# Optimization experiments

Measured on AMD Instinct MI355X. Metric: run time of the kernel, lower is better.

The kernel has to match this reference:

```python
import jax, jax.numpy as jnp
import numpy as np

B, E, F = 16384, 128, 6
ITEM_V, CATE_V, HIST = 91718, 11, 50
I_IDX, J_IDX = np.triu_indices(F, k=1)  # 15 field pairs, loop order (0,1),(0,2),...
EPS = 1e-5


def _xavier(key, shape):
    fan_in, fan_out = shape[0], shape[-1]
    std = (2.0 / (fan_in + fan_out)) ** 0.5
    return std * jax.random.normal(key, shape, dtype=jnp.float32)


def setup_inputs() -> dict:
    key = jax.random.key(0)
    ks = jax.random.split(key, 20)
    inp = {
        'item_id': jax.random.randint(ks[0], (B,), 0, ITEM_V),
        'item_emb_d128': jax.random.normal(ks[1], (B, 128), dtype=jnp.float32),
        'likes_level': jax.random.randint(ks[2], (B,), 0, CATE_V),
        'views_level': jax.random.randint(ks[3], (B,), 0, CATE_V),
        'item_seq': jax.random.randint(ks[4], (B, HIST), 0, ITEM_V),
        # learned parameters
        'item_emb': 0.05 * jax.random.normal(ks[5], (ITEM_V, E), dtype=jnp.float32),
        'cate_emb': 0.05 * jax.random.normal(ks[6], (CATE_V, E), dtype=jnp.float32),
        'mm_W': _xavier(ks[7], (128, E)), 'mm_b': jnp.zeros((E,), jnp.float32),
        'ln_g': jnp.ones((E,), jnp.float32), 'ln_b': jnp.zeros((E,), jnp.float32),
        'se_W1': _xavier(ks[8], (F, F // 2)), 'se_b1': jnp.zeros((F // 2,), jnp.float32),
        'se_W2': _xavier(ks[9], (F // 2, F)), 'se_b2': jnp.zeros((F,), jnp.float32),
        'bi_W': _xavier(ks[10], (E, E)),
        'mlp_W1': _xavier(ks[11], (21 * E, 512)), 'mlp_b1': jnp.zeros((512,), jnp.float32),
        'bn1_g': jnp.ones((512,), jnp.float32), 'bn1_b': jnp.zeros((512,), jnp.float32),
        'bn1_rm': jnp.zeros((512,), jnp.float32), 'bn1_rv': jnp.ones((512,), jnp.float32),
        'mlp_W2': _xavier(ks[12], (512, 256)), 'mlp_b2': jnp.zeros((256,), jnp.float32),
        'bn2_g': jnp.ones((256,), jnp.float32), 'bn2_b': jnp.zeros((256,), jnp.float32),
        'bn2_rm': jnp.zeros((256,), jnp.float32), 'bn2_rv': jnp.ones((256,), jnp.float32),
        'mlp_W3': _xavier(ks[13], (256, 1)), 'mlp_b3': jnp.zeros((1,), jnp.float32),
    }
    return inp


def _forward(item_id, item_emb_d128, likes_level, views_level, item_seq,
             item_emb, cate_emb, mm_W, mm_b, ln_g, ln_b,
             se_W1, se_b1, se_W2, se_b2, bi_W,
             mlp_W1, mlp_b1, bn1_g, bn1_b, bn1_rm, bn1_rv,
             mlp_W2, mlp_b2, bn2_g, bn2_b, bn2_rm, bn2_rv,
             mlp_W3, mlp_b3):
    b = item_id.shape[0]
    tab = item_emb.at[0].set(0.0)  # padding_idx=0
    like_feat = cate_emb[likes_level]
    view_feat = cate_emb[views_level]
    item_feat = tab[item_id]
    # mm_proj: Linear -> LayerNorm -> ReLU
    mm = item_emb_d128 @ mm_W + mm_b
    mu = mm.mean(-1, keepdims=True)
    var = jnp.var(mm, axis=-1, keepdims=True)
    mm = jax.nn.relu((mm - mu) / jnp.sqrt(var + EPS) * ln_g + ln_b)
    # masked mean pooling over history
    seq_emb = tab[item_seq]                               # (B, HIST, E)
    valid = (item_seq != 0).astype(seq_emb.dtype)
    seq_sum = (seq_emb * valid[..., None]).sum(1)
    cnt = jnp.clip(valid.sum(1, keepdims=True), 1.0)
    hist_feat = seq_sum / cnt
    user_feat = jnp.zeros((b, E), seq_emb.dtype)
    x = jnp.stack([user_feat, like_feat, view_feat, item_feat, mm, hist_feat], axis=1)  # (B,6,E)
    # SENet
    z = x.mean(-1)
    w = jax.nn.sigmoid(jax.nn.relu(z @ se_W1 + se_b1) @ se_W2 + se_b2)
    xs = x * w[:, :, None]
    # bilinear 'all'
    xw = jnp.einsum('bfe,ed->bfd', xs, bi_W)
    p = xs[:, I_IDX, :] * xw[:, J_IDX, :]                 # (B,15,E)
    c = jnp.concatenate([xs.reshape(b, -1), p.reshape(b, -1)], axis=1)  # (B, 2688)
    # MLP head (eval mode: BN uses running stats, dropout off)
    h = c @ mlp_W1 + mlp_b1
    h = jax.nn.relu((h - bn1_rm) / jnp.sqrt(bn1_rv + EPS) * bn1_g + bn1_b)
    h = h @ mlp_W2 + mlp_b2
    h = jax.nn.relu((h - bn2_rm) / jnp.sqrt(bn2_rv + EPS) * bn2_g + bn2_b)
    logits = h @ mlp_W3 + mlp_b3
    return jax.nn.sigmoid(logits)[:, 0]


def reference(item_id, item_emb_d128, likes_level, views_level, item_seq,
              item_emb, cate_emb, mm_W, mm_b, ln_g, ln_b,
              se_W1, se_b1, se_W2, se_b2, bi_W,
              mlp_W1, mlp_b1, bn1_g, bn1_b, bn1_rm, bn1_rv,
              mlp_W2, mlp_b2, bn2_g, bn2_b, bn2_rm, bn2_rv,
              mlp_W3, mlp_b3):
    return _forward(item_id, item_emb_d128, likes_level, views_level, item_seq,
                    item_emb, cate_emb, mm_W, mm_b, ln_g, ln_b,
                    se_W1, se_b1, se_W2, se_b2, bi_W,
                    mlp_W1, mlp_b1, bn1_g, bn1_b, bn1_rm, bn1_rv,
                    mlp_W2, mlp_b2, bn2_g, bn2_b, bn2_rm, bn2_rv,
                    mlp_W3, mlp_b3)
```

## Files before the change

kernel.cpp:

```cpp
#include <hip/hip_runtime.h>
#include <hip/hip_bf16.h>

typedef __hip_bfloat16 bfloat;
typedef __bf16 bf16x8 __attribute__((ext_vector_type(8)));
typedef float f32x4 __attribute__((ext_vector_type(4)));

#define B_SZ   16384
#define E_DIM  128
#define HIST_L 50


#define IPACK 0x3221110000ULL
#define JPACK 0x3323213210ULL

__device__ __forceinline__ void gl_lds16(const void* g, void* l) {
    __builtin_amdgcn_global_load_lds(
        (const __attribute__((address_space(1))) unsigned int*)g,
        (__attribute__((address_space(3))) unsigned int*)l, 16, 0, 0);
}

__device__ __forceinline__ bf16x8 mul_bf16x8(bf16x8 a, bf16x8 b) {
    union { bf16x8 v; __hip_bfloat162 h[4]; } ua, ub, ur;
    ua.v = a; ub.v = b;
    #pragma unroll
    for (int i = 0; i < 4; ++i) ur.h[i] = __hmul2(ua.h[i], ub.h[i]);
    return ur.v;
}

__global__ __launch_bounds__(256) void feat_kernel(
    const int* __restrict__ item_id,
    const int* __restrict__ likes, const int* __restrict__ views,
    const int* __restrict__ seq,
    const float* __restrict__ item_emb, const float* __restrict__ cate_emb,
    const float* __restrict__ mm,
    const float* __restrict__ ln_g, const float* __restrict__ ln_b,
    const float* __restrict__ se_W1, const float* __restrict__ se_b1,
    const float* __restrict__ se_W2, const float* __restrict__ se_b2,
    bfloat* __restrict__ xs)
{
    const int tid = threadIdx.x;
    const int r   = tid >> 7;
    const int e   = tid & 127;
    const int b   = blockIdx.x * 2 + r;
    const int w   = tid >> 6;

    __shared__ float redh[2][4][128];
    __shared__ int   seq_s[2][64];
    __shared__ float lnred[4], lnred2[4];
    __shared__ float zred[5][4];
    __shared__ float wsh[2][6];
    __shared__ int   cnt_s[2];

    if (e < 64) seq_s[r][e] = (e < HIST_L) ? seq[(size_t)b * HIST_L + e] : 0;
    __syncthreads();

    const int iid = item_id[b];
    const float like_v = cate_emb[likes[b] * 128 + e];
    const float view_v = cate_emb[views[b] * 128 + e];
    const float item_raw = item_emb[(size_t)iid * 128 + e];
    const float item_v = iid ? item_raw : 0.f;
    const float acc = mm[(size_t)b * 128 + e];

    const int q   = e >> 5;
    const int l32 = e & 31;
    float4 hs = make_float4(0.f, 0.f, 0.f, 0.f);
    #pragma unroll
    for (int g = 0; g < 13; ++g) {
        int s = seq_s[r][g * 4 + q];
        const float4 v = *(const float4*)&item_emb[(size_t)s * 128 + l32 * 4];
        float m = (s != 0) ? 1.f : 0.f;
        hs.x = fmaf(v.x, m, hs.x);
        hs.y = fmaf(v.y, m, hs.y);
        hs.z = fmaf(v.z, m, hs.z);
        hs.w = fmaf(v.w, m, hs.w);
    }

    {
        float v = acc;
        #pragma unroll
        for (int off = 32; off > 0; off >>= 1) v += __shfl_down(v, off, 64);
        if ((tid & 63) == 0) lnred[w] = v;
    }
    __syncthreads();
    const float mu = (lnred[2 * r] + lnred[2 * r + 1]) * (1.f / 128.f);
    const float d  = acc - mu;
    {
        float v = d * d;
        #pragma unroll
        for (int off = 32; off > 0; off >>= 1) v += __shfl_down(v, off, 64);
        if ((tid & 63) == 0) lnred2[w] = v;
    }
    redh[r][q][l32 * 4 + 0] = hs.x;
    redh[r][q][l32 * 4 + 1] = hs.y;
    redh[r][q][l32 * 4 + 2] = hs.z;
    redh[r][q][l32 * 4 + 3] = hs.w;
    if ((w & 1) == 0 && e < 64) {
        bool valid = (e < HIST_L) && (seq_s[r][e] != 0);
        unsigned long long m = __ballot(valid);
        if (e == 0) cnt_s[r] = (int)__popcll(m);
    }
    __syncthreads();
    const float var = (lnred2[2 * r] + lnred2[2 * r + 1]) * (1.f / 128.f);
    float xmm = d * rsqrtf(var + 1e-5f) * ln_g[e] + ln_b[e];
    xmm = fmaxf(xmm, 0.f);

    const int cnt = cnt_s[r] > 0 ? cnt_s[r] : 1;
    const float hist_v = (redh[r][0][e] + redh[r][1][e] +
                          redh[r][2][e] + redh[r][3][e]) / (float)cnt;

    {
        float s1 = like_v, s2 = view_v, s3 = item_v, s4 = xmm, s5 = hist_v;
        #pragma unroll
        for (int off = 32; off > 0; off >>= 1) {
            s1 += __shfl_down(s1, off, 64);
            s2 += __shfl_down(s2, off, 64);
            s3 += __shfl_down(s3, off, 64);
            s4 += __shfl_down(s4, off, 64);
            s5 += __shfl_down(s5, off, 64);
        }
        if ((tid & 63) == 0) {
            zred[0][w] = s1; zred[1][w] = s2; zred[2][w] = s3;
            zred[3][w] = s4; zred[4][w] = s5;
        }
    }
    __syncthreads();

    if (e == 0) {
        float z[6];
        z[0] = 0.f;
        #pragma unroll
        for (int f = 1; f < 6; ++f)
            z[f] = (zred[f - 1][2 * r] + zred[f - 1][2 * r + 1]) * (1.f / 128.f);
        float a[3];
        #pragma unroll
        for (int j = 0; j < 3; ++j) {
            float s = se_b1[j];
            #pragma unroll
            for (int f = 0; f < 6; ++f) s += z[f] * se_W1[f * 3 + j];
            a[j] = fmaxf(s, 0.f);
        }
        #pragma unroll
        for (int f = 0; f < 6; ++f) {
            float s = se_b2[f];
            #pragma unroll
            for (int j = 0; j < 3; ++j) s += a[j] * se_W2[j * 6 + f];
            wsh[r][f] = 1.f / (1.f + expf(-s));
        }
    }
    __syncthreads();

    bfloat* xrow = xs + (size_t)b * 640;
    xrow[0 * 128 + e] = __float2bfloat16(like_v * wsh[r][1]);
    xrow[1 * 128 + e] = __float2bfloat16(view_v * wsh[r][2]);
    xrow[2 * 128 + e] = __float2bfloat16(item_v * wsh[r][3]);
    xrow[3 * 128 + e] = __float2bfloat16(xmm    * wsh[r][4]);
    xrow[4 * 128 + e] = __float2bfloat16(hist_v * wsh[r][5]);
}

__global__ __launch_bounds__(256) void transpose_f32_bf16(
    const float* __restrict__ in, bfloat* __restrict__ out, int K, int N)
{
    int idx = blockIdx.x * 256 + threadIdx.x;
    if (idx < K * N) {
        int k = idx / N, n = idx % N;
        out[(size_t)n * K + k] = __float2bfloat16(in[idx]);
    }
}

__global__ __launch_bounds__(256) void transpose_W1c(
    const float* __restrict__ W1, bfloat* __restrict__ W1t)
{
    int idx = blockIdx.x * 256 + threadIdx.x;
    if (idx < 512 * 1920) {
        int n = idx / 1920, kk = idx % 1920;
        int orig = kk + (kk < 640 ? 128 : 768);
        W1t[idx] = __float2bfloat16(W1[(size_t)orig * 512 + n]);
    }
}

__global__ __launch_bounds__(256) void bn_pre(
    const float* __restrict__ lb1, const float* __restrict__ g1,
    const float* __restrict__ bb1, const float* __restrict__ rm1,
    const float* __restrict__ rv1,
    const float* __restrict__ lb2, const float* __restrict__ g2,
    const float* __restrict__ bb2, const float* __restrict__ rm2,
    const float* __restrict__ rv2,
    const float* __restrict__ mm_b,
    float* __restrict__ S1, float* __restrict__ T1,
    float* __restrict__ S2, float* __restrict__ T2,
    float* __restrict__ Tmm)
{
    int j = blockIdx.x * 256 + threadIdx.x;
    if (j < 512) {
        float s = g1[j] * rsqrtf(rv1[j] + 1e-5f);
        S1[j] = s;
        T1[j] = (lb1[j] - rm1[j]) * s + bb1[j];
    } else if (j < 768) {
        int k = j - 512;
        float s = g2[k] * rsqrtf(rv2[k] + 1e-5f);
        S2[k] = s;
        T2[k] = (lb2[k] - rm2[k]) * s + bb2[k];
    } else if (j < 896) {
        Tmm[j - 768] = mm_b[j - 768];
    }
}

template<int MODE, int EPI, int MT, int NT, int F32OUT>
__global__ __launch_bounds__(256) void gemm_bt(
    const void* __restrict__ A, const bfloat* __restrict__ A2,
    const bfloat* __restrict__ Bt, void* __restrict__ C,
    int M, int N, int K,
    const float* __restrict__ S, const float* __restrict__ T)
{
    __shared__ __align__(16) short As[2][MT * 64];
    __shared__ __align__(16) short Bs[2][NT * 64];

    const int tid  = threadIdx.x;
    const int bm   = blockIdx.x * MT;
    const int bn   = blockIdx.y * NT;
    const int wave = tid >> 6;
    const int lane = tid & 63;
    const int wm   = (wave >> 1) * (MT / 2);
    const int wn   = (wave & 1) * (NT / 2);
    constexpr int AF = MT / 32;
    constexpr int BF = NT / 32;

    const short* Ag  = (const short*)A;
    const short* A2g = (const short*)A2;
    const short* Bg  = (const short*)Bt;

    f32x4 acc[AF][BF];
    #pragma unroll
    for (int i = 0; i < AF; ++i)
        #pragma unroll
        for (int j = 0; j < BF; ++j)
            acc[i][j] = (f32x4){0.f, 0.f, 0.f, 0.f};

    const int srow = tid >> 3;
    const int sck  = tid & 7;

    auto stage = [&](int buf, int kt) {
        #pragma unroll
        for (int rr = 0; rr < NT / 32; ++rr) {
            int row = srow + rr * 32;
            int g   = sck ^ (row & 7);
            gl_lds16(&Bg[(long)(bn + row) * K + kt + g * 8],
                     &Bs[buf][row * 64 + sck * 8]);
        }
        if (MODE == 1 && kt >= 640) {
            #pragma unroll
            for (int rr = 0; rr < MT / 32; ++rr) {
                int row = srow + rr * 32;
                int g   = sck ^ (row & 7);
                int kg  = kt - 640 + g * 8;
                int pp  = kg >> 7;
                int isl = (int)((IPACK >> (4 * pp)) & 15);
                int jsl = (int)((JPACK >> (4 * pp)) & 15);
                int e0  = kg & 127;
                long rb = (long)(bm + row);
                bf16x8 a = *(const bf16x8*)&Ag [rb * 640 + isl * 128 + e0];
                bf16x8 b = *(const bf16x8*)&A2g[rb * 512 + jsl * 128 + e0];
                *(bf16x8*)&As[buf][row * 64 + sck * 8] = mul_bf16x8(a, b);
            }
        } else if (MODE == 3) {
            const float* Af = (const float*)A;
            #pragma unroll
            for (int rr = 0; rr < MT / 32; ++rr) {
                int row = srow + rr * 32;
                int g   = sck ^ (row & 7);
                long aoff = (long)(bm + row) * K + kt + g * 8;
                float4 f0 = *(const float4*)&Af[aoff];
                float4 f1 = *(const float4*)&Af[aoff + 4];
                union { bf16x8 v; unsigned short s[8]; } u;
                u.s[0] = __bfloat16_as_ushort(__float2bfloat16(f0.x));
                u.s[1] = __bfloat16_as_ushort(__float2bfloat16(f0.y));
                u.s[2] = __bfloat16_as_ushort(__float2bfloat16(f0.z));
                u.s[3] = __bfloat16_as_ushort(__float2bfloat16(f0.w));
                u.s[4] = __bfloat16_as_ushort(__float2bfloat16(f1.x));
                u.s[5] = __bfloat16_as_ushort(__float2bfloat16(f1.y));
                u.s[6] = __bfloat16_as_ushort(__float2bfloat16(f1.z));
                u.s[7] = __bfloat16_as_ushort(__float2bfloat16(f1.w));
                *(bf16x8*)&As[buf][row * 64 + sck * 8] = u.v;
            }
        } else {
            #pragma unroll
            for (int rr = 0; rr < MT / 32; ++rr) {
                int row = srow + rr * 32;
                int g   = sck ^ (row & 7);
                const short* src;
                if (MODE == 2) {
                    int gr = bm + row;
                    src = &Ag[((long)(gr >> 2)) * 640 +
                              ((gr & 3) + 1) * 128 + kt + g * 8];
                } else if (MODE == 1) {
                    src = &Ag[(long)(bm + row) * 640 + kt + g * 8];
                } else {
                    src = &Ag[(long)(bm + row) * K + kt + g * 8];
                }
                gl_lds16(src, &As[buf][row * 64 + sck * 8]);
            }
        }
    };

    const int rbase = lane & 15;
    const int cswz  = rbase & 7;

    const int nk = K >> 6;
    stage(0, 0);
    asm volatile("s_waitcnt vmcnt(0) lgkmcnt(0)" ::: "memory");
    __builtin_amdgcn_s_barrier();

    for (int i = 0; i < nk; ++i) {
        const int cur = i & 1;
        if (i + 1 < nk) stage(cur ^ 1, (i + 1) << 6);

        #pragma unroll
        for (int h = 0; h < 2; ++h) {
            const int cg = h * 4 + (lane >> 4);
            const int ca = (cg ^ cswz) << 3;
            bf16x8 af[AF], bfr[BF];
            #pragma unroll
            for (int mt = 0; mt < AF; ++mt)
                af[mt] = *(const bf16x8*)
                    &As[cur][(wm + mt * 16 + rbase) * 64 + ca];
            #pragma unroll
            for (int nt = 0; nt < BF; ++nt)
                bfr[nt] = *(const bf16x8*)
                    &Bs[cur][(wn + nt * 16 + rbase) * 64 + ca];
            #pragma unroll
            for (int mt = 0; mt < AF; ++mt)
                #pragma unroll
                for (int nt = 0; nt < BF; ++nt)
                    acc[mt][nt] = __builtin_amdgcn_mfma_f32_16x16x32_bf16(
                        af[mt], bfr[nt], acc[mt][nt], 0, 0, 0);
        }

        if (i + 1 < nk) {
            asm volatile("s_waitcnt vmcnt(0) lgkmcnt(0)" ::: "memory");
            __builtin_amdgcn_s_barrier();
        }
    }

    const int col0 = lane & 15;
    const int row0 = (lane >> 4) * 4;
    #pragma unroll
    for (int nt = 0; nt < BF; ++nt) {
        int col = bn + wn + nt * 16 + col0;
        float s = 1.f, t = 0.f;
        if (EPI) { s = (EPI == 1) ? S[col] : 1.f; t = T[col]; }
        #pragma unroll
        for (int mt = 0; mt < AF; ++mt) {
            #pragma unroll
            for (int i = 0; i < 4; ++i) {
                int row = bm + wm + mt * 16 + row0 + i;
                float v = acc[mt][nt][i];
                if (EPI == 1) v = fmaxf(v * s + t, 0.f);
                if (EPI == 2) v = v + t;
                if (F32OUT) ((float*)C)[(size_t)row * N + col] = v;
                else ((bfloat*)C)[(size_t)row * N + col] = __float2bfloat16(v);
            }
        }
    }
}

__global__ __launch_bounds__(256) void head_kernel(
    const bfloat* __restrict__ h2, const float* __restrict__ W3,
    const float* __restrict__ b3, float* __restrict__ out)
{
    int lane = threadIdx.x & 63;
    int row  = blockIdx.x * 4 + (threadIdx.x >> 6);
    float acc = 0.f;
    #pragma unroll
    for (int i = 0; i < 4; ++i)
        acc += __bfloat162float(h2[(size_t)row * 256 + i * 64 + lane]) *
               W3[i * 64 + lane];
    #pragma unroll
    for (int off = 32; off > 0; off >>= 1) acc += __shfl_down(acc, off, 64);
    if (lane == 0) {
        float l = acc + b3[0];
        out[row] = 1.f / (1.f + expf(-l));
    }
}

extern "C" void kernel_launch(void* const* d_in, const int* in_sizes, int n_in,
                              void* d_out, int out_size, void* d_ws, size_t ws_size,
                              hipStream_t stream) {
    const int*   item_id = (const int*)  d_in[0];
    const float* d128    = (const float*)d_in[1];
    const int*   likes   = (const int*)  d_in[2];
    const int*   views   = (const int*)  d_in[3];
    const int*   seq     = (const int*)  d_in[4];
    const float* item_emb= (const float*)d_in[5];
    const float* cate_emb= (const float*)d_in[6];
    const float* mm_W    = (const float*)d_in[7];
    const float* mm_b    = (const float*)d_in[8];
    const float* ln_g    = (const float*)d_in[9];
    const float* ln_b    = (const float*)d_in[10];
    const float* se_W1   = (const float*)d_in[11];
    const float* se_b1   = (const float*)d_in[12];
    const float* se_W2   = (const float*)d_in[13];
    const float* se_b2   = (const float*)d_in[14];
    const float* bi_W    = (const float*)d_in[15];
    const float* W1      = (const float*)d_in[16];
    const float* b1      = (const float*)d_in[17];
    const float* bn1_g   = (const float*)d_in[18];
    const float* bn1_b   = (const float*)d_in[19];
    const float* bn1_rm  = (const float*)d_in[20];
    const float* bn1_rv  = (const float*)d_in[21];
    const float* W2      = (const float*)d_in[22];
    const float* b2      = (const float*)d_in[23];
    const float* bn2_g   = (const float*)d_in[24];
    const float* bn2_b   = (const float*)d_in[25];
    const float* bn2_rm  = (const float*)d_in[26];
    const float* bn2_rv  = (const float*)d_in[27];
    const float* W3      = (const float*)d_in[28];
    const float* b3      = (const float*)d_in[29];

    const size_t fixed = 2300416;
    int CH = 1024;
    if      (fixed + (size_t)16384 * 3328 <= ws_size) CH = 16384;
    else if (fixed + (size_t)8192  * 3328 <= ws_size) CH = 8192;
    else if (fixed + (size_t)4096  * 3328 <= ws_size) CH = 4096;
    else if (fixed + (size_t)2048  * 3328 <= ws_size) CH = 2048;

    char* ws = (char*)d_ws;
    bfloat* W1t = (bfloat*)(ws);
    bfloat* W2t = (bfloat*)(ws + 1966080);
    bfloat* bWt = (bfloat*)(ws + 2228224);
    bfloat* mmWt= (bfloat*)(ws + 2260992);
    float*  S1  = (float*) (ws + 2293760);
    float*  T1  = (float*) (ws + 2295808);
    float*  S2  = (float*) (ws + 2297856);
    float*  T2  = (float*) (ws + 2298880);
    float*  Tmm = (float*) (ws + 2299904);
    bfloat* xs  = (bfloat*)(ws + fixed);
    bfloat* xw  = (bfloat*)(ws + fixed + (size_t)CH * 1280);
    bfloat* h1  = (bfloat*)(ws + fixed + (size_t)CH * 2304);
    bfloat* h2  = xw;
    float*  mm  = (float*)h1;

    transpose_W1c<<<(512 * 1920 + 255) / 256, 256, 0, stream>>>(W1, W1t);
    transpose_f32_bf16<<<(512 * 256 + 255) / 256, 256, 0, stream>>>(W2, W2t, 512, 256);
    transpose_f32_bf16<<<(128 * 128 + 255) / 256, 256, 0, stream>>>(bi_W, bWt, 128, 128);
    transpose_f32_bf16<<<(128 * 128 + 255) / 256, 256, 0, stream>>>(mm_W, mmWt, 128, 128);
    bn_pre<<<4, 256, 0, stream>>>(b1, bn1_g, bn1_b, bn1_rm, bn1_rv,
                                  b2, bn2_g, bn2_b, bn2_rm, bn2_rv,
                                  mm_b, S1, T1, S2, T2, Tmm);

    for (int off = 0; off < B_SZ; off += CH) {
        dim3 gmm(CH / 128, 128 / 64);
        gemm_bt<3, 2, 128, 64, 1><<<gmm, 256, 0, stream>>>(
            d128 + (size_t)off * 128, nullptr, mmWt, mm,
            CH, 128, 128, nullptr, Tmm);

        feat_kernel<<<CH / 2, 256, 0, stream>>>(
            item_id + off, likes + off, views + off,
            seq + (size_t)off * HIST_L, item_emb, cate_emb, mm,
            ln_g, ln_b, se_W1, se_b1, se_W2, se_b2, xs);

        dim3 gxw(CH * 4 / 128, 128 / 64);
        gemm_bt<2, 0, 128, 64, 0><<<gxw, 256, 0, stream>>>(
            xs, nullptr, bWt, xw, CH * 4, 128, 128, nullptr, nullptr);

        dim3 g1(CH / 128, 512 / 64);
        gemm_bt<1, 1, 128, 64, 0><<<g1, 256, 0, stream>>>(
            xs, xw, W1t, h1, CH, 512, 1920, S1, T1);

        dim3 g2(CH / 128, 256 / 64);
        gemm_bt<0, 1, 128, 64, 0><<<g2, 256, 0, stream>>>(
            h1, nullptr, W2t, h2, CH, 256, 512, S2, T2);

        head_kernel<<<CH / 4, 256, 0, stream>>>(h2, W3, b3, (float*)d_out + off);
    }
}
```

Measured before the change: 315.2 us.

## Materialize pair products and f32->bf16 input, use 3-stage 64x64 GEMM pipeline

The GEMM is rebuilt around 64x64 tiles with a three-buffer LDS pipeline, so loads run two K-steps ahead with a partial vmcnt wait instead of a full drain each iteration. Bilinear pair products and the fp32->bf16 conversion of the dense input move into standalone kernels, which lets every GEMM A-operand load go through async global->LDS copies instead of in-register compute. The cost is extra global writes and reads for the pair buffer (CH*2560 bytes) and the converted input, two more kernel launches, and a larger workspace that may force smaller chunks.

```diff
diff --git a/kernel.cpp b/kernel.cpp
--- a/kernel.cpp
+++ b/kernel.cpp
@@ -176,6 +176,41 @@
         int orig = kk + (kk < 640 ? 128 : 768);
         W1t[idx] = __float2bfloat16(W1[(size_t)orig * 512 + n]);
     }
+}
+
+__global__ __launch_bounds__(256) void cvt_f32_bf16(
+    const float* __restrict__ in, bfloat* __restrict__ out, int n8)
+{
+    int idx = blockIdx.x * 256 + threadIdx.x;
+    if (idx < n8) {
+        float4 f0 = ((const float4*)in)[idx * 2];
+        float4 f1 = ((const float4*)in)[idx * 2 + 1];
+        union { bf16x8 v; unsigned short s[8]; } u;
+        u.s[0] = __bfloat16_as_ushort(__float2bfloat16(f0.x));
+        u.s[1] = __bfloat16_as_ushort(__float2bfloat16(f0.y));
+        u.s[2] = __bfloat16_as_ushort(__float2bfloat16(f0.z));
+        u.s[3] = __bfloat16_as_ushort(__float2bfloat16(f0.w));
+        u.s[4] = __bfloat16_as_ushort(__float2bfloat16(f1.x));
+        u.s[5] = __bfloat16_as_ushort(__float2bfloat16(f1.y));
+        u.s[6] = __bfloat16_as_ushort(__float2bfloat16(f1.z));
+        u.s[7] = __bfloat16_as_ushort(__float2bfloat16(f1.w));
+        ((bf16x8*)out)[idx] = u.v;
+    }
+}
+
+__global__ __launch_bounds__(256) void pair_kernel(
+    const bfloat* __restrict__ xs, const bfloat* __restrict__ xw,
+    bfloat* __restrict__ P, int total)
+{
+    int idx = blockIdx.x * 256 + threadIdx.x;
+    if (idx >= total) return;
+    int b = idx / 160, c = idx % 160;
+    int pp = c >> 4, q = c & 15;
+    int isl = (int)((IPACK >> (4 * pp)) & 15);
+    int jsl = (int)((JPACK >> (4 * pp)) & 15);
+    bf16x8 a = *(const bf16x8*)&xs[(size_t)b * 640 + isl * 128 + q * 8];
+    bf16x8 w = *(const bf16x8*)&xw[((size_t)b * 4 + jsl) * 128 + q * 8];
+    *(bf16x8*)&P[(size_t)b * 1280 + c * 8] = mul_bf16x8(a, w);
 }
 
 __global__ __launch_bounds__(256) void bn_pre(
@@ -205,35 +240,33 @@
     }
 }
 
-template<int MODE, int EPI, int MT, int NT, int F32OUT>
+template<int MODE, int EPI, int F32OUT>
 __global__ __launch_bounds__(256) void gemm_bt(
     const void* __restrict__ A, const bfloat* __restrict__ A2,
     const bfloat* __restrict__ Bt, void* __restrict__ C,
     int M, int N, int K,
     const float* __restrict__ S, const float* __restrict__ T)
 {
-    __shared__ __align__(16) short As[2][MT * 64];
-    __shared__ __align__(16) short Bs[2][NT * 64];
+    __shared__ __align__(16) short As[3][64 * 64];
+    __shared__ __align__(16) short Bs[3][64 * 64];
 
     const int tid  = threadIdx.x;
-    const int bm   = blockIdx.x * MT;
-    const int bn   = blockIdx.y * NT;
+    const int bm   = blockIdx.x * 64;
+    const int bn   = blockIdx.y * 64;
     const int wave = tid >> 6;
     const int lane = tid & 63;
-    const int wm   = (wave >> 1) * (MT / 2);
-    const int wn   = (wave & 1) * (NT / 2);
-    constexpr int AF = MT / 32;
-    constexpr int BF = NT / 32;
+    const int wm   = (wave >> 1) * 32;
+    const int wn   = (wave & 1) * 32;
 
     const short* Ag  = (const short*)A;
     const short* A2g = (const short*)A2;
     const short* Bg  = (const short*)Bt;
 
-    f32x4 acc[AF][BF];
-    #pragma unroll
-    for (int i = 0; i < AF; ++i)
-        #pragma unroll
-        for (int j = 0; j < BF; ++j)
+    f32x4 acc[2][2];
+    #pragma unroll
+    for (int i = 0; i < 2; ++i)
+        #pragma unroll
+        for (int j = 0; j < 2; ++j)
             acc[i][j] = (f32x4){0.f, 0.f, 0.f, 0.f};
 
     const int srow = tid >> 3;
@@ -241,64 +274,30 @@
 
     auto stage = [&](int buf, int kt) {
         #pragma unroll
-        for (int rr = 0; rr < NT / 32; ++rr) {
+        for (int rr = 0; rr < 2; ++rr) {
             int row = srow + rr * 32;
             int g   = sck ^ (row & 7);
             gl_lds16(&Bg[(long)(bn + row) * K + kt + g * 8],
                      &Bs[buf][row * 64 + sck * 8]);
         }
-        if (MODE == 1 && kt >= 640) {
-            #pragma unroll
-            for (int rr = 0; rr < MT / 32; ++rr) {
-                int row = srow + rr * 32;
-                int g   = sck ^ (row & 7);
-                int kg  = kt - 640 + g * 8;
-                int pp  = kg >> 7;
-                int isl = (int)((IPACK >> (4 * pp)) & 15);
-                int jsl = (int)((JPACK >> (4 * pp)) & 15);
-                int e0  = kg & 127;
+        #pragma unroll
+        for (int rr = 0; rr < 2; ++rr) {
+            int row = srow + rr * 32;
+            int g   = sck ^ (row & 7);
+            const short* src;
+            if (MODE == 4) {
                 long rb = (long)(bm + row);
-                bf16x8 a = *(const bf16x8*)&Ag [rb * 640 + isl * 128 + e0];
-                bf16x8 b = *(const bf16x8*)&A2g[rb * 512 + jsl * 128 + e0];
-                *(bf16x8*)&As[buf][row * 64 + sck * 8] = mul_bf16x8(a, b);
+                src = (kt < 640)
+                    ? &Ag [rb * 640  + kt + g * 8]
+                    : &A2g[rb * 1280 + (kt - 640) + g * 8];
+            } else if (MODE == 2) {
+                int gr = bm + row;
+                src = &Ag[((long)(gr >> 2)) * 640 +
+                          ((gr & 3) + 1) * 128 + kt + g * 8];
+            } else {
+                src = &Ag[(long)(bm + row) * K + kt + g * 8];
             }
-        } else if (MODE == 3) {
-            const float* Af = (const float*)A;
-            #pragma unroll
-            for (int rr = 0; rr < MT / 32; ++rr) {
-                int row = srow + rr * 32;
-                int g   = sck ^ (row & 7);
-                long aoff = (long)(bm + row) * K + kt + g * 8;
-                float4 f0 = *(const float4*)&Af[aoff];
-                float4 f1 = *(const float4*)&Af[aoff + 4];
-                union { bf16x8 v; unsigned short s[8]; } u;
-                u.s[0] = __bfloat16_as_ushort(__float2bfloat16(f0.x));
-                u.s[1] = __bfloat16_as_ushort(__float2bfloat16(f0.y));
-                u.s[2] = __bfloat16_as_ushort(__float2bfloat16(f0.z));
-                u.s[3] = __bfloat16_as_ushort(__float2bfloat16(f0.w));
-                u.s[4] = __bfloat16_as_ushort(__float2bfloat16(f1.x));
-                u.s[5] = __bfloat16_as_ushort(__float2bfloat16(f1.y));
-                u.s[6] = __bfloat16_as_ushort(__float2bfloat16(f1.z));
-                u.s[7] = __bfloat16_as_ushort(__float2bfloat16(f1.w));
-                *(bf16x8*)&As[buf][row * 64 + sck * 8] = u.v;
-            }
-        } else {
-            #pragma unroll
-            for (int rr = 0; rr < MT / 32; ++rr) {
-                int row = srow + rr * 32;
-                int g   = sck ^ (row & 7);
-                const short* src;
-                if (MODE == 2) {
-                    int gr = bm + row;
-                    src = &Ag[((long)(gr >> 2)) * 640 +
-                              ((gr & 3) + 1) * 128 + kt + g * 8];
-                } else if (MODE == 1) {
-                    src = &Ag[(long)(bm + row) * 640 + kt + g * 8];
-                } else {
-                    src = &Ag[(long)(bm + row) * K + kt + g * 8];
-                }
-                gl_lds16(src, &As[buf][row * 64 + sck * 8]);
-            }
+            gl_lds16(src, &As[buf][row * 64 + sck * 8]);
         }
     };
 
@@ -307,49 +306,48 @@
 
     const int nk = K >> 6;
     stage(0, 0);
-    asm volatile("s_waitcnt vmcnt(0) lgkmcnt(0)" ::: "memory");
-    __builtin_amdgcn_s_barrier();
+    stage(1, 64);
 
     for (int i = 0; i < nk; ++i) {
-        const int cur = i & 1;
-        if (i + 1 < nk) stage(cur ^ 1, (i + 1) << 6);
-
+        if (i + 1 < nk) asm volatile("s_waitcnt vmcnt(4)" ::: "memory");
+        else            asm volatile("s_waitcnt vmcnt(0)" ::: "memory");
+        __builtin_amdgcn_s_barrier();
+        __builtin_amdgcn_sched_barrier(0);
+
+        const int cur = i % 3;
         #pragma unroll
         for (int h = 0; h < 2; ++h) {
             const int cg = h * 4 + (lane >> 4);
             const int ca = (cg ^ cswz) << 3;
-            bf16x8 af[AF], bfr[BF];
-            #pragma unroll
-            for (int mt = 0; mt < AF; ++mt)
+            bf16x8 af[2], bfr[2];
+            #pragma unroll
+            for (int mt = 0; mt < 2; ++mt)
                 af[mt] = *(const bf16x8*)
                     &As[cur][(wm + mt * 16 + rbase) * 64 + ca];
             #pragma unroll
-            for (int nt = 0; nt < BF; ++nt)
+            for (int nt = 0; nt < 2; ++nt)
                 bfr[nt] = *(const bf16x8*)
                     &Bs[cur][(wn + nt * 16 + rbase) * 64 + ca];
             #pragma unroll
-            for (int mt = 0; mt < AF; ++mt)
+            for (int mt = 0; mt < 2; ++mt)
                 #pragma unroll
-                for (int nt = 0; nt < BF; ++nt)
+                for (int nt = 0; nt < 2; ++nt)
                     acc[mt][nt] = __builtin_amdgcn_mfma_f32_16x16x32_bf16(
                         af[mt], bfr[nt], acc[mt][nt], 0, 0, 0);
         }
 
-        if (i + 1 < nk) {
-            asm volatile("s_waitcnt vmcnt(0) lgkmcnt(0)" ::: "memory");
-            __builtin_amdgcn_s_barrier();
-        }
+        if (i + 2 < nk) stage((i + 2) % 3, (i + 2) << 6);
     }
 
     const int col0 = lane & 15;
     const int row0 = (lane >> 4) * 4;
     #pragma unroll
-    for (int nt = 0; nt < BF; ++nt) {
+    for (int nt = 0; nt < 2; ++nt) {
         int col = bn + wn + nt * 16 + col0;
         float s = 1.f, t = 0.f;
         if (EPI) { s = (EPI == 1) ? S[col] : 1.f; t = T[col]; }
         #pragma unroll
-        for (int mt = 0; mt < AF; ++mt) {
+        for (int mt = 0; mt < 2; ++mt) {
             #pragma unroll
             for (int i = 0; i < 4; ++i) {
                 int row = bm + wm + mt * 16 + row0 + i;
@@ -418,10 +416,10 @@
 
     const size_t fixed = 2300416;
     int CH = 1024;
-    if      (fixed + (size_t)16384 * 3328 <= ws_size) CH = 16384;
-    else if (fixed + (size_t)8192  * 3328 <= ws_size) CH = 8192;
-    else if (fixed + (size_t)4096  * 3328 <= ws_size) CH = 4096;
-    else if (fixed + (size_t)2048  * 3328 <= ws_size) CH = 2048;
+    if      (fixed + (size_t)16384 * 5120 <= ws_size) CH = 16384;
+    else if (fixed + (size_t)8192  * 5120 <= ws_size) CH = 8192;
+    else if (fixed + (size_t)4096  * 5120 <= ws_size) CH = 4096;
+    else if (fixed + (size_t)2048  * 5120 <= ws_size) CH = 2048;
 
     char* ws = (char*)d_ws;
     bfloat* W1t = (bfloat*)(ws);
@@ -435,9 +433,11 @@
     float*  Tmm = (float*) (ws + 2299904);
     bfloat* xs  = (bfloat*)(ws + fixed);
     bfloat* xw  = (bfloat*)(ws + fixed + (size_t)CH * 1280);
-    bfloat* h1  = (bfloat*)(ws + fixed + (size_t)CH * 2304);
-    bfloat* h2  = xw;
-    float*  mm  = (float*)h1;
+    bfloat* h1  = xw;
+    bfloat* P   = (bfloat*)(ws + fixed + (size_t)CH * 2304);
+    float*  mm  = (float*)P;
+    bfloat* h2  = (bfloat*)P;
+    bfloat* d128b = (bfloat*)(ws + fixed + (size_t)CH * 4864);
 
     transpose_W1c<<<(512 * 1920 + 255) / 256, 256, 0, stream>>>(W1, W1t);
     transpose_f32_bf16<<<(512 * 256 + 255) / 256, 256, 0, stream>>>(W2, W2t, 512, 256);
@@ -448,26 +448,31 @@
                                   mm_b, S1, T1, S2, T2, Tmm);
 
     for (int off = 0; off < B_SZ; off += CH) {
-        dim3 gmm(CH / 128, 128 / 64);
-        gemm_bt<3, 2, 128, 64, 1><<<gmm, 256, 0, stream>>>(
-            d128 + (size_t)off * 128, nullptr, mmWt, mm,
-            CH, 128, 128, nullptr, Tmm);
+        cvt_f32_bf16<<<(CH * 16 + 255) / 256, 256, 0, stream>>>(
+            d128 + (size_t)off * 128, d128b, CH * 16);
+
+        dim3 gmm(CH / 64, 2);
+        gemm_bt<0, 2, 1><<<gmm, 256, 0, stream>>>(
+            d128b, nullptr, mmWt, mm, CH, 128, 128, nullptr, Tmm);
 
         feat_kernel<<<CH / 2, 256, 0, stream>>>(
             item_id + off, likes + off, views + off,
             seq + (size_t)off * HIST_L, item_emb, cate_emb, mm,
             ln_g, ln_b, se_W1, se_b1, se_W2, se_b2, xs);
 
-        dim3 gxw(CH * 4 / 128, 128 / 64);
-        gemm_bt<2, 0, 128, 64, 0><<<gxw, 256, 0, stream>>>(
+        dim3 gxw(CH * 4 / 64, 2);
+        gemm_bt<2, 0, 0><<<gxw, 256, 0, stream>>>(
             xs, nullptr, bWt, xw, CH * 4, 128, 128, nullptr, nullptr);
 
-        dim3 g1(CH / 128, 512 / 64);
-        gemm_bt<1, 1, 128, 64, 0><<<g1, 256, 0, stream>>>(
-            xs, xw, W1t, h1, CH, 512, 1920, S1, T1);
-
-        dim3 g2(CH / 128, 256 / 64);
-        gemm_bt<0, 1, 128, 64, 0><<<g2, 256, 0, stream>>>(
+        pair_kernel<<<(CH * 160 + 255) / 256, 256, 0, stream>>>(
+            xs, xw, P, CH * 160);
+
+        dim3 g1(CH / 64, 8);
+        gemm_bt<4, 1, 0><<<g1, 256, 0, stream>>>(
+            xs, P, W1t, h1, CH, 512, 1920, S1, T1);
+
+        dim3 g2(CH / 64, 4);
+        gemm_bt<0, 1, 0><<<g2, 256, 0, stream>>>(
             h1, nullptr, W2t, h2, CH, 256, 512, S2, T2);
 
         head_kernel<<<CH / 4, 256, 0, stream>>>(h2, W3, b3, (float*)d_out + off);
```

Measured after the change: 314.6 us. No clear change (-0.2%).
